# Kernel tuning notes

Hardware: AMD Instinct MI355X
Metric: run time of the kernel (lower is better)

The kernel has to match this reference:

```python
import math
import jax, jax.numpy as jnp
import numpy as np

B, T, C = 2, 2048, 4096
H = 32
D = C // H  # head_dim = 128


def compute_freq(dim, max_len, theta=10000):
    freq = 1.0 / theta ** (jnp.arange(0, dim, 2, dtype=jnp.float32) / dim)
    t = jnp.arange(max_len, dtype=jnp.float32)
    m = jnp.einsum('i,j->ij', t, freq)          # [L, dim/2]
    m = jnp.concatenate([m, m], axis=-1)         # [L, dim]
    return jnp.cos(m), jnp.sin(m)


def rotate_half(x):
    # Faithful to source: depth = full last dim, so x1 is the whole tensor
    # and x2 is empty -> rotate_half(x) == x (a quirk of the original code).
    depth = x.shape[-1]
    x1 = x[..., :depth]
    x2 = x[..., depth:]
    return jnp.concatenate([-x2, x1], axis=-1)


def setup_inputs() -> dict:
    key = jax.random.key(0)
    kx, kq, kk, kv, ko = jax.random.split(key, 5)
    std = 0.02
    input_ids = jax.random.normal(kx, (B, T, C), dtype=jnp.float32)
    Wq = jax.random.normal(kq, (C, C), dtype=jnp.float32) * std
    Wk = jax.random.normal(kk, (C, C), dtype=jnp.float32) * std
    Wv = jax.random.normal(kv, (C, C), dtype=jnp.float32) * std
    Wo = jax.random.normal(ko, (C, C), dtype=jnp.float32) * std
    # Additive causal mask, as typically passed to this module.
    causal = jnp.tril(jnp.ones((T, T), dtype=bool))
    attention_mask = jnp.where(causal, 0.0, -1e9).astype(jnp.float32)[None, None]
    return {"input_ids": input_ids, "Wq": Wq, "Wk": Wk, "Wv": Wv,
            "Wo": Wo, "attention_mask": attention_mask}


def reference(input_ids, Wq, Wk, Wv, Wo, attention_mask):
    b, t, c = input_ids.shape
    # QKV projections (no bias), reshape to [b, h, t, d]
    q = (input_ids @ Wq).reshape(b, t, H, D).swapaxes(1, 2)
    k = (input_ids @ Wk).reshape(b, t, H, D).swapaxes(1, 2)
    v = (input_ids @ Wv).reshape(b, t, H, D).swapaxes(1, 2)
    # Inline RoPE (faithful, including the source's rotate_half behavior)
    cos, sin = compute_freq(D, t)                # [t, D]
    q = q * cos + rotate_half(q) * sin
    k = k * cos + rotate_half(k) * sin
    # Naive full attention
    attn = jnp.einsum('bhqd,bhkd->bhqk', q, k) / math.sqrt(D)
    attn = attn + attention_mask
    attn = jax.nn.softmax(attn, axis=-1)
    out = jnp.einsum('bhqk,bhkd->bhqd', attn, v)
    out = out.swapaxes(1, 2).reshape(b, t, c)
    return out @ Wo
```

## Files before the change

kernel.cpp:

```cpp
#include <hip/hip_runtime.h>
#include <hip/hip_bf16.h>

#define B_ 2
#define T_ 2048
#define C_ 4096
#define H_ 32
#define D_ 128

typedef __bf16 bf16x8 __attribute__((ext_vector_type(8)));
typedef float f32x4 __attribute__((ext_vector_type(4)));

__device__ __forceinline__ void gload_lds16(const void* g, void* l) {
  __builtin_amdgcn_global_load_lds(
      (const __attribute__((address_space(1))) void*)g,
      (__attribute__((address_space(3))) void*)l, 16, 0, 0);
}

__device__ __forceinline__ ushort f2bf(float f) {
  union { float f; uint u; } x; x.f = f;
  uint r = x.u + 0x7FFFu + ((x.u >> 16) & 1u);
  return (ushort)(r >> 16);
}

__global__ __launch_bounds__(256) void cvt_f32_bf16(
    const float* __restrict__ in, ushort* __restrict__ out)
{
  long i = ((long)blockIdx.x * 256 + threadIdx.x) * 8;
  float4 a = *(const float4*)&in[i];
  float4 b = *(const float4*)&in[i + 4];
  union { ushort u[8]; uint4 v; } g;
  g.u[0] = f2bf(a.x); g.u[1] = f2bf(a.y); g.u[2] = f2bf(a.z); g.u[3] = f2bf(a.w);
  g.u[4] = f2bf(b.x); g.u[5] = f2bf(b.y); g.u[6] = f2bf(b.z); g.u[7] = f2bf(b.w);
  *(uint4*)&out[i] = g.v;
}

__global__ __launch_bounds__(256) void transpose_f32_bf16(
    const float* __restrict__ in, ushort* __restrict__ out, int ldi, int ldo)
{
  __shared__ __align__(16) ushort tile[64][72];
  const float* ip = in + (long)blockIdx.y * 64 * ldi + (long)blockIdx.x * 64;
  ushort* op = out + (long)blockIdx.x * 64 * ldo + (long)blockIdx.y * 64;
  const int t = threadIdx.x;
  const int row = t >> 2, c0 = (t & 3) * 16;
#pragma unroll
  for (int v = 0; v < 4; ++v) {
    float4 f = *(const float4*)&ip[(long)row * ldi + c0 + v * 4];
    ushort4 w;
    w.x = f2bf(f.x); w.y = f2bf(f.y); w.z = f2bf(f.z); w.w = f2bf(f.w);
    *(ushort4*)&tile[row][c0 + v * 4] = w;
  }
  __syncthreads();
#pragma unroll
  for (int i = 0; i < 2; ++i) {
    int t2 = i * 256 + t;
    int orow = t2 >> 3, ch = t2 & 7;
    union { ushort u[8]; uint4 v; } g;
#pragma unroll
    for (int e = 0; e < 8; ++e) g.u[e] = tile[ch * 8 + e][orow];
    *(uint4*)&op[(long)orow * ldo + ch * 8] = g.v;
  }
}

__global__ __launch_bounds__(256) void transpose_bf16(
    const ushort* __restrict__ in, ushort* __restrict__ out,
    int ldi, int ldo, long zi1, long zi2, long zo1, long zo2)
{
  __shared__ __align__(16) ushort tile[64][72];
  const int z = blockIdx.z;
  const long z1 = z & 31, z2 = z >> 5;
  const ushort* ip = in + z1 * zi1 + z2 * zi2 +
                     (long)blockIdx.y * 64 * ldi + (long)blockIdx.x * 64;
  ushort* op = out + z1 * zo1 + z2 * zo2 +
               (long)blockIdx.x * 64 * ldo + (long)blockIdx.y * 64;
  const int t = threadIdx.x;
#pragma unroll
  for (int i = 0; i < 2; ++i) {
    int t2 = i * 256 + t;
    int row = t2 >> 3, ch = t2 & 7;
    *(uint4*)&tile[row][ch * 8] = *(const uint4*)&ip[(long)row * ldi + ch * 8];
  }
  __syncthreads();
#pragma unroll
  for (int i = 0; i < 2; ++i) {
    int t2 = i * 256 + t;
    int orow = t2 >> 3, ch = t2 & 7;
    union { ushort u[8]; uint4 v; } g;
#pragma unroll
    for (int e = 0; e < 8; ++e) g.u[e] = tile[ch * 8 + e][orow];
    *(uint4*)&op[(long)orow * ldo + ch * 8] = g.v;
  }
}

#define STAGE_A(h, tt) do {                                                    \
    __hip_bfloat16* dst_ = AS + ((((tt) & 1) * 2 + (h)) * 8192) + w * 512;     \
    const __hip_bfloat16* src_ = Asrc + (size_t)((h) * 128) * K + (size_t)(tt) * 64; \
    gload_lds16(src_, dst_);                                                   \
    gload_lds16(src_ + (size_t)64 * K, dst_ + 4096);                           \
  } while (0)

#define STAGE_B(h, tt) do {                                                    \
    __hip_bfloat16* dst_ = BS + ((((tt) & 1) * 2 + (h)) * 8192) + w * 512;     \
    const __hip_bfloat16* src_ = Bsrc + (size_t)((h) * 128) * K + (size_t)(tt) * 64; \
    gload_lds16(src_, dst_);                                                   \
    gload_lds16(src_ + (size_t)64 * K, dst_ + 4096);                           \
  } while (0)

template <typename OutT>
__global__ __launch_bounds__(512, 2) void gemm256(
    const __hip_bfloat16* __restrict__ A,
    const __hip_bfloat16* __restrict__ Bt,
    OutT* __restrict__ C,
    int M, int N, int K, int rope_mode)
{
  extern __shared__ __hip_bfloat16 smem[];
  __hip_bfloat16* AS = smem;
  __hip_bfloat16* BS = smem + 32768;

  const int tid = threadIdx.x, lane = tid & 63, w = tid >> 6;
  const int wm = w >> 2, wn = w & 3;
  const int fr = lane & 15, quad = lane >> 4;

  const int bid = blockIdx.x;
  const int s = (bid & 7) * 32 + (bid >> 3);
  const int m0 = (s >> 4) * 256, n0 = (s & 15) * 256;

  const int srow = tid >> 3;
  const int schunk = ((tid & 7) ^ (srow & 7)) * 8;
  const __hip_bfloat16* Asrc = A + (size_t)(m0 + srow) * K + schunk;
  const __hip_bfloat16* Bsrc = Bt + (size_t)(n0 + srow) * K + schunk;

  f32x4 acc[2][2][4][2] = {};

  STAGE_A(0, 0); STAGE_B(0, 0); STAGE_A(1, 0); STAGE_B(1, 0);
  STAGE_A(0, 1); STAGE_B(1, 1);
  asm volatile("s_waitcnt vmcnt(4)" ::: "memory");
  asm volatile("s_barrier" ::: "memory");

  const int NT = K >> 6;
  for (int t = 0; t < NT; ++t) {
    const int cb = t & 1;
    const __hip_bfloat16* As0 = AS + cb * 16384;
    const __hip_bfloat16* Bs0 = BS + cb * 16384;
    bf16x8 afrag[4][2], bfrag[2][2];
#pragma unroll
    for (int ph = 0; ph < 4; ++ph) {
      const int pM = ph >> 1;
      const int pN = (ph >> 1) ^ (ph & 1);
      if (ph == 0 || ph == 2) {
        const __hip_bfloat16* base = As0 + pM * 8192;
#pragma unroll
        for (int mf = 0; mf < 4; ++mf) {
          const int row = wm * 64 + mf * 16 + fr;
#pragma unroll
          for (int ks = 0; ks < 2; ++ks)
            afrag[mf][ks] = *(const bf16x8*)
                &base[row * 64 + (((ks * 4 + quad) ^ (fr & 7)) << 3)];
        }
      }
      if (ph != 2) {
        const __hip_bfloat16* base = Bs0 + pN * 8192;
#pragma unroll
        for (int nf = 0; nf < 2; ++nf) {
          const int row = wn * 32 + nf * 16 + fr;
#pragma unroll
          for (int ks = 0; ks < 2; ++ks)
            bfrag[nf][ks] = *(const bf16x8*)
                &base[row * 64 + (((ks * 4 + quad) ^ (fr & 7)) << 3)];
        }
      }
      if (ph == 0)      { if (t + 1 < NT) STAGE_A(1, t + 1); }
      else if (ph == 1) { if (t + 1 < NT) STAGE_B(0, t + 1); }
      else if (ph == 2) { if (t + 2 < NT) STAGE_A(0, t + 2); }
      else {
        if (t + 2 < NT) STAGE_B(1, t + 2);
        if (t < NT - 2) asm volatile("s_waitcnt vmcnt(4)" ::: "memory");
        else            asm volatile("s_waitcnt vmcnt(0)" ::: "memory");
      }
      asm volatile("s_barrier" ::: "memory");
      asm volatile("s_waitcnt lgkmcnt(0)" ::: "memory");
      __builtin_amdgcn_sched_barrier(0);
      __builtin_amdgcn_s_setprio(1);
#pragma unroll
      for (int mf = 0; mf < 4; ++mf)
#pragma unroll
        for (int nf = 0; nf < 2; ++nf)
#pragma unroll
          for (int ks = 0; ks < 2; ++ks)
            acc[pM][pN][mf][nf] = __builtin_amdgcn_mfma_f32_16x16x32_bf16(
                afrag[mf][ks], bfrag[nf][ks], acc[pM][pN][mf][nf], 0, 0, 0);
      __builtin_amdgcn_s_setprio(0);
      __builtin_amdgcn_sched_barrier(0);
      asm volatile("s_barrier" ::: "memory");
    }
  }

  const float gscale = (rope_mode == 1) ? 0.08838834764831845f : 1.0f;
  float freqv[2] = {0.f, 0.f};
  if (rope_mode) {
#pragma unroll
    for (int nf = 0; nf < 2; ++nf)
      freqv[nf] = exp2f((float)((wn & 1) * 32 + nf * 16 + fr) *
                        -0.20762050593046012f);
  }
#pragma unroll
  for (int pM = 0; pM < 2; ++pM)
#pragma unroll
    for (int mf = 0; mf < 4; ++mf)
#pragma unroll
      for (int r = 0; r < 4; ++r) {
        const int grow = m0 + pM * 128 + wm * 64 + mf * 16 + quad * 4 + r;
        float fct[2] = {1.f, 1.f};
        if (rope_mode) {
          const int tt = grow & (T_ - 1);
#pragma unroll
          for (int nf = 0; nf < 2; ++nf) {
            float sn, cs;
            sincosf((float)tt * freqv[nf], &sn, &cs);
            fct[nf] = (cs + sn) * gscale;
          }
        }
#pragma unroll
        for (int pN = 0; pN < 2; ++pN)
#pragma unroll
          for (int nf = 0; nf < 2; ++nf) {
            const int col = n0 + pN * 128 + wn * 32 + nf * 16 + fr;
            float v = acc[pM][pN][mf][nf][r] * fct[nf];
            if constexpr (sizeof(OutT) == 4)
              C[(size_t)grow * N + col] = v;
            else
              C[(size_t)grow * N + col] = __float2bfloat16(v);
          }
      }
}

__global__ __launch_bounds__(256, 2) void flash_attn(
    const __hip_bfloat16* __restrict__ Q,
    const __hip_bfloat16* __restrict__ K,
    const __hip_bfloat16* __restrict__ Vt,
    __hip_bfloat16* __restrict__ O)
{
  __shared__ __align__(16) __hip_bfloat16 Ks[128 * 128];
  __shared__ __align__(16) __hip_bfloat16 Ps[4][32 * 128];
  const int tid = threadIdx.x, lane = tid & 63, wid = tid >> 6;
  const int bx = blockIdx.x, bh = blockIdx.y;
  const int b = bh >> 5, h = bh & 31;
  const int fr = lane & 15, fq = (lane >> 4) * 8;
  const int quad = lane >> 4;
  const __hip_bfloat16* Kbase = K + (size_t)(b * T_) * C_ + h * D_;
  const __hip_bfloat16* Vbase = Vt + (size_t)bh * D_ * T_;

  const int strow = wid * 32 + quad;

  for (int pass = 0; pass < 2; ++pass) {
    const int qt = pass ? (15 - bx) : bx;
    const int q0 = qt * 128;
    const __hip_bfloat16* Qbase = Q + (size_t)(b * T_ + q0) * C_ + h * D_;

#pragma unroll
    for (int j = 0; j < 8; ++j) {
      const int swz = quad + (j & 1) * 4;
      gload_lds16(Qbase + (size_t)(strow + j * 4) * C_ + ((fr ^ swz) * 8),
                  &Ks[(wid * 8 + j) * 512]);
    }
    __syncthreads();
    bf16x8 qf[2][4];
#pragma unroll
    for (int mi = 0; mi < 2; ++mi)
#pragma unroll
      for (int ks = 0; ks < 4; ++ks)
        qf[mi][ks] = *(const bf16x8*)&Ks[(wid * 32 + mi * 16 + fr) * 128 +
                                         (((ks * 4 + quad) ^ (fr & 7)) << 3)];
    __syncthreads();

    float m_i[2][4], l_i[2][4];
#pragma unroll
    for (int mi = 0; mi < 2; ++mi)
#pragma unroll
      for (int r = 0; r < 4; ++r) { m_i[mi][r] = -1e30f; l_i[mi][r] = 0.f; }
    f32x4 oa[2][8] = {};

    for (int kt = 0; kt <= qt; ++kt) {
#pragma unroll
      for (int j = 0; j < 8; ++j) {
        const int swz = quad + (j & 1) * 4;
        gload_lds16(
            Kbase + (size_t)(kt * 128 + strow + j * 4) * C_ + ((fr ^ swz) * 8),
            &Ks[(wid * 8 + j) * 512]);
      }
      __syncthreads();

      f32x4 s[2][8] = {};
#pragma unroll
      for (int ks = 0; ks < 4; ++ks) {
        bf16x8 kf[8];
#pragma unroll
        for (int ni = 0; ni < 8; ++ni)
          kf[ni] = *(const bf16x8*)&Ks[(ni * 16 + fr) * 128 +
                                       (((ks * 4 + quad) ^ (fr & 7)) << 3)];
#pragma unroll
        for (int mi = 0; mi < 2; ++mi)
#pragma unroll
          for (int ni = 0; ni < 8; ++ni)
            s[mi][ni] = __builtin_amdgcn_mfma_f32_16x16x32_bf16(
                qf[mi][ks], kf[ni], s[mi][ni], 0, 0, 0);
      }
      __syncthreads();

#pragma unroll
      for (int j = 0; j < 8; ++j) {
        const int swz = quad + (j & 1) * 4;
        gload_lds16(
            Vbase + (size_t)(strow + j * 4) * T_ + kt * 128 + ((fr ^ swz) * 8),
            &Ks[(wid * 8 + j) * 512]);
      }

      if (kt == qt) {
#pragma unroll
        for (int mi = 0; mi < 2; ++mi)
#pragma unroll
          for (int ni = 0; ni < 8; ++ni)
#pragma unroll
            for (int r = 0; r < 4; ++r) {
              int rl = wid * 32 + mi * 16 + quad * 4 + r;
              int cl = ni * 16 + fr;
              if (cl > rl) s[mi][ni][r] = -1e30f;
            }
      }

#pragma unroll
      for (int mi = 0; mi < 2; ++mi)
#pragma unroll
        for (int r = 0; r < 4; ++r) {
          float mx = -1e30f;
#pragma unroll
          for (int ni = 0; ni < 8; ++ni) mx = fmaxf(mx, s[mi][ni][r]);
          mx = fmaxf(mx, __shfl_xor(mx, 1, 16));
          mx = fmaxf(mx, __shfl_xor(mx, 2, 16));
          mx = fmaxf(mx, __shfl_xor(mx, 4, 16));
          mx = fmaxf(mx, __shfl_xor(mx, 8, 16));
          float mnew = fmaxf(m_i[mi][r], mx);
          float alpha = __expf(m_i[mi][r] - mnew);
          float rs = 0.f;
#pragma unroll
          for (int ni = 0; ni < 8; ++ni) {
            float p = __expf(s[mi][ni][r] - mnew);
            s[mi][ni][r] = p;
            rs += p;
          }
          rs += __shfl_xor(rs, 1, 16);
          rs += __shfl_xor(rs, 2, 16);
          rs += __shfl_xor(rs, 4, 16);
          rs += __shfl_xor(rs, 8, 16);
          m_i[mi][r] = mnew;
          l_i[mi][r] = l_i[mi][r] * alpha + rs;
#pragma unroll
          for (int ni = 0; ni < 8; ++ni) oa[mi][ni][r] *= alpha;
        }

#pragma unroll
      for (int mi = 0; mi < 2; ++mi)
#pragma unroll
        for (int ni = 0; ni < 8; ++ni) {
          const int sw = (ni ^ (mi * 4 + quad)) & 7;
#pragma unroll
          for (int r = 0; r < 4; ++r)
            Ps[wid][(mi * 16 + quad * 4 + r) * 128 + sw * 16 + fr] =
                __float2bfloat16(s[mi][ni][r]);
        }
      __syncthreads();

#pragma unroll
      for (int ks = 0; ks < 4; ++ks) {
        bf16x8 pf[2], vf[8];
#pragma unroll
        for (int mi = 0; mi < 2; ++mi) {
          const int rowl = mi * 16 + fr;
          const int sw = ((ks * 2 + (quad >> 1)) ^ ((rowl >> 2) & 7)) & 7;
          pf[mi] = *(const bf16x8*)&Ps[wid][rowl * 128 + sw * 16 + (quad & 1) * 8];
        }
#pragma unroll
        for (int ni = 0; ni < 8; ++ni)
          vf[ni] = *(const bf16x8*)&Ks[(ni * 16 + fr) * 128 +
                                       (((ks * 4 + quad) ^ (fr & 7)) << 3)];
#pragma unroll
        for (int mi = 0; mi < 2; ++mi)
#pragma unroll
          for (int ni = 0; ni < 8; ++ni)
            oa[mi][ni] = __builtin_amdgcn_mfma_f32_16x16x32_bf16(
                pf[mi], vf[ni], oa[mi][ni], 0, 0, 0);
      }
      __syncthreads();
    }

#pragma unroll
    for (int mi = 0; mi < 2; ++mi)
#pragma unroll
      for (int r = 0; r < 4; ++r) {
        float inv = 1.f / l_i[mi][r];
        int grow = b * T_ + q0 + wid * 32 + mi * 16 + quad * 4 + r;
#pragma unroll
        for (int ni = 0; ni < 8; ++ni)
          O[(size_t)grow * C_ + h * D_ + ni * 16 + fr] =
              __float2bfloat16(oa[mi][ni][r] * inv);
      }
  }
}

extern "C" void kernel_launch(void* const* d_in, const int* in_sizes, int n_in,
                              void* d_out, int out_size, void* d_ws, size_t ws_size,
                              hipStream_t stream) {
  const float* X  = (const float*)d_in[0];
  const float* Wq = (const float*)d_in[1];
  const float* Wk = (const float*)d_in[2];
  const float* Wv = (const float*)d_in[3];
  const float* Wo = (const float*)d_in[4];
  float* out = (float*)d_out;

  char* ws = (char*)d_ws;
  const size_t SZ = (size_t)4096 * 4096 * 2;
  __hip_bfloat16* Xb  = (__hip_bfloat16*)(ws);
  __hip_bfloat16* Wt  = (__hip_bfloat16*)(ws + SZ);
  __hip_bfloat16* Qb  = (__hip_bfloat16*)(ws + 2 * SZ);
  __hip_bfloat16* Kb  = (__hip_bfloat16*)(ws + 3 * SZ);
  __hip_bfloat16* Vb  = (__hip_bfloat16*)(ws + 4 * SZ);
  __hip_bfloat16* Vtb = Xb;
  __hip_bfloat16* Ob  = Vb;

  const dim3 blk(256);
  const dim3 gT(64, 64, 1);

  hipFuncSetAttribute(reinterpret_cast<const void*>(&gemm256<__hip_bfloat16>),
                      hipFuncAttributeMaxDynamicSharedMemorySize, 131072);
  hipFuncSetAttribute(reinterpret_cast<const void*>(&gemm256<float>),
                      hipFuncAttributeMaxDynamicSharedMemorySize, 131072);

  cvt_f32_bf16<<<8192, blk, 0, stream>>>(X, (ushort*)Xb);

  transpose_f32_bf16<<<gT, blk, 0, stream>>>(Wq, (ushort*)Wt, 4096, 4096);
  gemm256<__hip_bfloat16><<<dim3(256), dim3(512), 131072, stream>>>(
      Xb, Wt, Qb, 4096, 4096, 4096, 1);
  transpose_f32_bf16<<<gT, blk, 0, stream>>>(Wk, (ushort*)Wt, 4096, 4096);
  gemm256<__hip_bfloat16><<<dim3(256), dim3(512), 131072, stream>>>(
      Xb, Wt, Kb, 4096, 4096, 4096, 2);
  transpose_f32_bf16<<<gT, blk, 0, stream>>>(Wv, (ushort*)Wt, 4096, 4096);
  gemm256<__hip_bfloat16><<<dim3(256), dim3(512), 131072, stream>>>(
      Xb, Wt, Vb, 4096, 4096, 4096, 0);

  transpose_bf16<<<dim3(2, 32, 64), blk, 0, stream>>>(
      (const ushort*)Vb, (ushort*)Vtb, 4096, 2048,
       128,  8388608,  262144,  8388608);

  flash_attn<<<dim3(8, 64), blk, 0, stream>>>(Qb, Kb, Vtb, Ob);

  transpose_f32_bf16<<<gT, blk, 0, stream>>>(Wo, (ushort*)Wt, 4096, 4096);
  gemm256<float><<<dim3(256), dim3(512), 131072, stream>>>(
      Ob, Wt, out, 4096, 4096, 4096, 0);
}
```

Baseline: 1.027 ms.

## Reorder GEMM phases for fragment reuse, add lazy softmax rescale and MFMA priority

The GEMM main loop is rewritten to prefetch all four half-tiles two steps ahead and walk the four quadrant MFMA groups in the order (0,0),(0,1),(1,1),(1,0). This lets A and B fragments be reused across phases and cuts LDS fragment reads per tile. The attention kernel skips the running-max rescale (alpha multiply on the output accumulator) unless some row's max grows by more than 6 over the stored max, trading exactness bounds for fewer exps and multiplies. It also raises wave priority around the attention MFMA blocks; the lazy-max path risks fp32 overflow only in extreme score ranges.

```diff
diff --git a/kernel.cpp b/kernel.cpp
--- a/kernel.cpp
+++ b/kernel.cpp
@@ -105,6 +105,16 @@
     gload_lds16(src_ + (size_t)64 * K, dst_ + 4096);                           \
   } while (0)
 
+#define MFMA16(pM, pN, AF, BF)                                                 \
+  _Pragma("unroll")                                                            \
+  for (int mf = 0; mf < 4; ++mf)                                               \
+    _Pragma("unroll")                                                          \
+    for (int nf = 0; nf < 2; ++nf)                                             \
+      _Pragma("unroll")                                                        \
+      for (int ks = 0; ks < 2; ++ks)                                           \
+        acc[pM][pN][mf][nf] = __builtin_amdgcn_mfma_f32_16x16x32_bf16(         \
+            AF[mf][ks], BF[nf][ks], acc[pM][pN][mf][nf], 0, 0, 0);
+
 template <typename OutT>
 __global__ __launch_bounds__(512, 2) void gemm256(
     const __hip_bfloat16* __restrict__ A,
@@ -132,66 +142,87 @@
   f32x4 acc[2][2][4][2] = {};
 
   STAGE_A(0, 0); STAGE_B(0, 0); STAGE_A(1, 0); STAGE_B(1, 0);
-  STAGE_A(0, 1); STAGE_B(1, 1);
-  asm volatile("s_waitcnt vmcnt(4)" ::: "memory");
+  STAGE_A(0, 1); STAGE_B(0, 1); STAGE_A(1, 1); STAGE_B(1, 1);
+  asm volatile("s_waitcnt vmcnt(8)" ::: "memory");
   asm volatile("s_barrier" ::: "memory");
 
   const int NT = K >> 6;
   for (int t = 0; t < NT; ++t) {
-    const int cb = t & 1;
-    const __hip_bfloat16* As0 = AS + cb * 16384;
-    const __hip_bfloat16* Bs0 = BS + cb * 16384;
-    bf16x8 afrag[4][2], bfrag[2][2];
-#pragma unroll
-    for (int ph = 0; ph < 4; ++ph) {
-      const int pM = ph >> 1;
-      const int pN = (ph >> 1) ^ (ph & 1);
-      if (ph == 0 || ph == 2) {
-        const __hip_bfloat16* base = As0 + pM * 8192;
-#pragma unroll
-        for (int mf = 0; mf < 4; ++mf) {
-          const int row = wm * 64 + mf * 16 + fr;
-#pragma unroll
-          for (int ks = 0; ks < 2; ++ks)
-            afrag[mf][ks] = *(const bf16x8*)
-                &base[row * 64 + (((ks * 4 + quad) ^ (fr & 7)) << 3)];
-        }
-      }
-      if (ph != 2) {
-        const __hip_bfloat16* base = Bs0 + pN * 8192;
-#pragma unroll
-        for (int nf = 0; nf < 2; ++nf) {
-          const int row = wn * 32 + nf * 16 + fr;
-#pragma unroll
-          for (int ks = 0; ks < 2; ++ks)
-            bfrag[nf][ks] = *(const bf16x8*)
-                &base[row * 64 + (((ks * 4 + quad) ^ (fr & 7)) << 3)];
-        }
-      }
-      if (ph == 0)      { if (t + 1 < NT) STAGE_A(1, t + 1); }
-      else if (ph == 1) { if (t + 1 < NT) STAGE_B(0, t + 1); }
-      else if (ph == 2) { if (t + 2 < NT) STAGE_A(0, t + 2); }
-      else {
-        if (t + 2 < NT) STAGE_B(1, t + 2);
-        if (t < NT - 2) asm volatile("s_waitcnt vmcnt(4)" ::: "memory");
-        else            asm volatile("s_waitcnt vmcnt(0)" ::: "memory");
-      }
-      asm volatile("s_barrier" ::: "memory");
-      asm volatile("s_waitcnt lgkmcnt(0)" ::: "memory");
-      __builtin_amdgcn_sched_barrier(0);
-      __builtin_amdgcn_s_setprio(1);
-#pragma unroll
-      for (int mf = 0; mf < 4; ++mf)
-#pragma unroll
-        for (int nf = 0; nf < 2; ++nf)
-#pragma unroll
-          for (int ks = 0; ks < 2; ++ks)
-            acc[pM][pN][mf][nf] = __builtin_amdgcn_mfma_f32_16x16x32_bf16(
-                afrag[mf][ks], bfrag[nf][ks], acc[pM][pN][mf][nf], 0, 0, 0);
-      __builtin_amdgcn_s_setprio(0);
-      __builtin_amdgcn_sched_barrier(0);
-      asm volatile("s_barrier" ::: "memory");
+    const __hip_bfloat16* As0 = AS + (t & 1) * 16384;
+    const __hip_bfloat16* Bs0 = BS + (t & 1) * 16384;
+    bf16x8 af[4][2], b0[2][2], b1[2][2];
+
+#pragma unroll
+    for (int mf = 0; mf < 4; ++mf) {
+      const int row = wm * 64 + mf * 16 + fr;
+#pragma unroll
+      for (int ks = 0; ks < 2; ++ks)
+        af[mf][ks] = *(const bf16x8*)
+            &As0[row * 64 + (((ks * 4 + quad) ^ (fr & 7)) << 3)];
     }
+#pragma unroll
+    for (int nf = 0; nf < 2; ++nf) {
+      const int row = wn * 32 + nf * 16 + fr;
+#pragma unroll
+      for (int ks = 0; ks < 2; ++ks)
+        b0[nf][ks] = *(const bf16x8*)
+            &Bs0[row * 64 + (((ks * 4 + quad) ^ (fr & 7)) << 3)];
+    }
+    asm volatile("s_barrier" ::: "memory");
+    asm volatile("s_waitcnt lgkmcnt(0)" ::: "memory");
+    __builtin_amdgcn_sched_barrier(0);
+    __builtin_amdgcn_s_setprio(1);
+    MFMA16(0, 0, af, b0)
+    __builtin_amdgcn_s_setprio(0);
+    __builtin_amdgcn_sched_barrier(0);
+    asm volatile("s_barrier" ::: "memory");
+
+#pragma unroll
+    for (int nf = 0; nf < 2; ++nf) {
+      const int row = wn * 32 + nf * 16 + fr;
+#pragma unroll
+      for (int ks = 0; ks < 2; ++ks)
+        b1[nf][ks] = *(const bf16x8*)
+            &Bs0[8192 + row * 64 + (((ks * 4 + quad) ^ (fr & 7)) << 3)];
+    }
+    if (t + 2 < NT) { STAGE_B(0, t + 2); STAGE_A(0, t + 2); }
+    asm volatile("s_barrier" ::: "memory");
+    asm volatile("s_waitcnt lgkmcnt(0)" ::: "memory");
+    __builtin_amdgcn_sched_barrier(0);
+    __builtin_amdgcn_s_setprio(1);
+    MFMA16(0, 1, af, b1)
+    __builtin_amdgcn_s_setprio(0);
+    __builtin_amdgcn_sched_barrier(0);
+    asm volatile("s_barrier" ::: "memory");
+
+#pragma unroll
+    for (int mf = 0; mf < 4; ++mf) {
+      const int row = wm * 64 + mf * 16 + fr;
+#pragma unroll
+      for (int ks = 0; ks < 2; ++ks)
+        af[mf][ks] = *(const bf16x8*)
+            &As0[8192 + row * 64 + (((ks * 4 + quad) ^ (fr & 7)) << 3)];
+    }
+    if (t + 2 < NT) STAGE_B(1, t + 2);
+    asm volatile("s_barrier" ::: "memory");
+    asm volatile("s_waitcnt lgkmcnt(0)" ::: "memory");
+    __builtin_amdgcn_sched_barrier(0);
+    __builtin_amdgcn_s_setprio(1);
+    MFMA16(1, 1, af, b1)
+    __builtin_amdgcn_s_setprio(0);
+    __builtin_amdgcn_sched_barrier(0);
+    asm volatile("s_barrier" ::: "memory");
+
+    if (t + 2 < NT) STAGE_A(1, t + 2);
+    if (t < NT - 2) asm volatile("s_waitcnt vmcnt(8)" ::: "memory");
+    else            asm volatile("s_waitcnt vmcnt(0)" ::: "memory");
+    asm volatile("s_barrier" ::: "memory");
+    __builtin_amdgcn_sched_barrier(0);
+    __builtin_amdgcn_s_setprio(1);
+    MFMA16(1, 0, af, b0)
+    __builtin_amdgcn_s_setprio(0);
+    __builtin_amdgcn_sched_barrier(0);
+    asm volatile("s_barrier" ::: "memory");
   }
 
   const float gscale = (rope_mode == 1) ? 0.08838834764831845f : 1.0f;
@@ -297,12 +328,14 @@
         for (int ni = 0; ni < 8; ++ni)
           kf[ni] = *(const bf16x8*)&Ks[(ni * 16 + fr) * 128 +
                                        (((ks * 4 + quad) ^ (fr & 7)) << 3)];
+        __builtin_amdgcn_s_setprio(1);
 #pragma unroll
         for (int mi = 0; mi < 2; ++mi)
 #pragma unroll
           for (int ni = 0; ni < 8; ++ni)
             s[mi][ni] = __builtin_amdgcn_mfma_f32_16x16x32_bf16(
                 qf[mi][ks], kf[ni], s[mi][ni], 0, 0, 0);
+        __builtin_amdgcn_s_setprio(0);
       }
       __syncthreads();
 
@@ -327,6 +360,8 @@
             }
       }
 
+      float mx_[2][4];
+      bool need = false;
 #pragma unroll
       for (int mi = 0; mi < 2; ++mi)
 #pragma unroll
@@ -338,24 +373,52 @@
           mx = fmaxf(mx, __shfl_xor(mx, 2, 16));
           mx = fmaxf(mx, __shfl_xor(mx, 4, 16));
           mx = fmaxf(mx, __shfl_xor(mx, 8, 16));
-          float mnew = fmaxf(m_i[mi][r], mx);
-          float alpha = __expf(m_i[mi][r] - mnew);
-          float rs = 0.f;
-#pragma unroll
-          for (int ni = 0; ni < 8; ++ni) {
-            float p = __expf(s[mi][ni][r] - mnew);
-            s[mi][ni][r] = p;
-            rs += p;
+          mx_[mi][r] = mx;
+          need = need || (mx > m_i[mi][r] + 6.0f);
+        }
+      if (__any(need)) {
+#pragma unroll
+        for (int mi = 0; mi < 2; ++mi)
+#pragma unroll
+          for (int r = 0; r < 4; ++r) {
+            float mnew = fmaxf(m_i[mi][r], mx_[mi][r]);
+            float alpha = __expf(m_i[mi][r] - mnew);
+            float rs = 0.f;
+#pragma unroll
+            for (int ni = 0; ni < 8; ++ni) {
+              float p = __expf(s[mi][ni][r] - mnew);
+              s[mi][ni][r] = p;
+              rs += p;
+            }
+            rs += __shfl_xor(rs, 1, 16);
+            rs += __shfl_xor(rs, 2, 16);
+            rs += __shfl_xor(rs, 4, 16);
+            rs += __shfl_xor(rs, 8, 16);
+            m_i[mi][r] = mnew;
+            l_i[mi][r] = l_i[mi][r] * alpha + rs;
+#pragma unroll
+            for (int ni = 0; ni < 8; ++ni) oa[mi][ni][r] *= alpha;
           }
-          rs += __shfl_xor(rs, 1, 16);
-          rs += __shfl_xor(rs, 2, 16);
-          rs += __shfl_xor(rs, 4, 16);
-          rs += __shfl_xor(rs, 8, 16);
-          m_i[mi][r] = mnew;
-          l_i[mi][r] = l_i[mi][r] * alpha + rs;
-#pragma unroll
-          for (int ni = 0; ni < 8; ++ni) oa[mi][ni][r] *= alpha;
-        }
+      } else {
+#pragma unroll
+        for (int mi = 0; mi < 2; ++mi)
+#pragma unroll
+          for (int r = 0; r < 4; ++r) {
+            float m0v = m_i[mi][r];
+            float rs = 0.f;
+#pragma unroll
+            for (int ni = 0; ni < 8; ++ni) {
+              float p = __expf(s[mi][ni][r] - m0v);
+              s[mi][ni][r] = p;
+              rs += p;
+            }
+            rs += __shfl_xor(rs, 1, 16);
+            rs += __shfl_xor(rs, 2, 16);
+            rs += __shfl_xor(rs, 4, 16);
+            rs += __shfl_xor(rs, 8, 16);
+            l_i[mi][r] += rs;
+          }
+      }
 
 #pragma unroll
       for (int mi = 0; mi < 2; ++mi)
@@ -382,12 +445,14 @@
         for (int ni = 0; ni < 8; ++ni)
           vf[ni] = *(const bf16x8*)&Ks[(ni * 16 + fr) * 128 +
                                        (((ks * 4 + quad) ^ (fr & 7)) << 3)];
+        __builtin_amdgcn_s_setprio(1);
 #pragma unroll
         for (int mi = 0; mi < 2; ++mi)
 #pragma unroll
           for (int ni = 0; ni < 8; ++ni)
             oa[mi][ni] = __builtin_amdgcn_mfma_f32_16x16x32_bf16(
                 pf[mi], vf[ni], oa[mi][ni], 0, 0, 0);
+        __builtin_amdgcn_s_setprio(0);
       }
       __syncthreads();
     }
```

After: 1.302 ms. +26.8%, slower.
